# Performance work log

Hardware: AMD Instinct MI355X
Metric: run time of the kernel (lower is better)

The kernel has to match this reference:

```python
import jax, jax.numpy as jnp
import numpy as np

IN_FEATURES = 1024
OUT_FEATURES = 1024
KNOT_COUNT = 5
ORDER = 3
BATCH = 4096


def setup_inputs() -> dict:
    key = jax.random.key(0)
    k1, k2 = jax.random.split(key)
    x = jax.random.normal(k1, (BATCH, IN_FEATURES), dtype=jnp.float32)
    knots = jnp.linspace(-1.0, 1.0, KNOT_COUNT, dtype=jnp.float32)
    coeffs = jax.random.normal(k2, (KNOT_COUNT + ORDER, OUT_FEATURES, IN_FEATURES), dtype=jnp.float32)
    return {"x": x, "knots": knots, "coeffs": coeffs}


def _bspline_bases(x, knots, order):
    # x: [B, I]; knots: [K] uniform grid. Extend to K + 2*order + 1 knots so
    # the number of degree-`order` basis functions is K + order.
    h = knots[1] - knots[0]
    left = knots[0] + h * jnp.arange(-order, 0, dtype=knots.dtype)
    right = knots[-1] + h * jnp.arange(1, order + 2, dtype=knots.dtype)
    t = jnp.concatenate([left, knots, right])  # [K + 2*order + 1]
    xe = x[..., None]  # [B, I, 1]
    # degree-0 indicator bases: [B, I, m-1]
    bases = ((xe >= t[:-1]) & (xe < t[1:])).astype(x.dtype)
    # Cox-de Boor recursion up to degree `order` (vectorized over batch/features)
    for k in range(1, order + 1):
        left_num = (xe - t[: -(k + 1)]) / (t[k:-1] - t[: -(k + 1)])
        right_num = (t[k + 1:] - xe) / (t[k + 1:] - t[1:-k])
        bases = left_num * bases[..., :-1] + right_num * bases[..., 1:]
    return bases  # [B, I, K + order]


def reference(x, knots, coeffs):
    # Faithful fused version of the per-(i,j) python loops:
    # spline_j(b) = sum_n B_n(x[b,i]) * coeffs[n, j, i]; output sums over i.
    bases = _bspline_bases(x, knots, ORDER)          # [B, I, N]
    return jnp.einsum('bin,noi->bo', bases, coeffs)  # [B, O]
```

## Files before the change

### kernel.cpp

```cpp
#include <hip/hip_runtime.h>
#include <hip/hip_bf16.h>
#include <cstdint>
#include <cstddef>

#define IN_F   1024
#define OUT_F  1024
#define NB     8
#define BATCH  4096
#define KTOT   (NB * IN_F)

typedef __attribute__((ext_vector_type(4))) float  f32x4;
typedef __attribute__((ext_vector_type(8))) float  f32x8;
typedef __attribute__((ext_vector_type(8))) __bf16 bf16x8;
typedef __attribute__((ext_vector_type(4))) unsigned short u16x4;

#define GLDS16(g, l)                                                     \
    __builtin_amdgcn_global_load_lds(                                    \
        (const __attribute__((address_space(1))) void*)(g),              \
        (__attribute__((address_space(3))) void*)(l), 16, 0, 0)

__device__ __forceinline__ void spline_w(float r, float w[4]) {
    const float r2 = r * r, r3 = r2 * r;
    const float omr = 1.0f - r;
    w[0] = omr * omr * omr * (1.0f / 6.0f);
    w[1] = (3.0f * r3 - 6.0f * r2 + 4.0f) * (1.0f / 6.0f);
    w[2] = (-3.0f * r3 + 3.0f * r2 + 3.0f * r + 1.0f) * (1.0f / 6.0f);
    w[3] = r3 * (1.0f / 6.0f);
}

__global__ void k_cvt(const float* __restrict__ src, __bf16* __restrict__ dst) {
    const size_t g   = blockIdx.x * blockDim.x + threadIdx.x;
    const size_t idx = g * 8;
    const int i = (int)(idx & 1023);
    const int o = (int)((idx >> 10) & 1023);
    const int c = (i >> 3) & 7;
    const int isw = (i & ~63) | ((c ^ (o & 7)) << 3);
    f32x8 v = *(const f32x8*)(src + idx);
    bf16x8 ov = __builtin_convertvector(v, bf16x8);
    *(bf16x8*)(dst + (idx - i) + isw) = ov;
}

__global__ void k_basis(const float* __restrict__ x, __bf16* __restrict__ A) {
    const int g    = blockIdx.x * blockDim.x + threadIdx.x;
    const int flat = g * 4;
    const int b = flat >> 10, i = flat & 1023;
    f32x4 xv = *(const f32x4*)(x + flat);

    float w[4][4];
    int   jj[4];
#pragma unroll
    for (int e = 0; e < 4; ++e) {
        const float u  = (xv[e] + 2.5f) * 2.0f;
        const float jf = floorf(u);
        jj[e] = (int)jf;
        spline_w(u - jf, w[e]);
    }

    const int c   = (i >> 3) & 7;
    const int isw = (i & ~63) | ((c ^ (b & 7)) << 3) | (i & 7);
    __bf16* base = A + (size_t)b * KTOT + isw;
#pragma unroll
    for (int n = 0; n < NB; ++n) {
        u16x4 pack;
#pragma unroll
        for (int e = 0; e < 4; ++e) {
            const int d = n - jj[e] + 3;
            float v = (d == 0) ? w[e][0]
                    : (d == 1) ? w[e][1]
                    : (d == 2) ? w[e][2]
                    : (d == 3) ? w[e][3] : 0.0f;
            __bf16 h = (__bf16)v;
            pack[e] = __builtin_bit_cast(unsigned short, h);
        }
        *(u16x4*)(base + n * IN_F) = pack;
    }
}

#define BM 256
#define BN 128
#define BK 64
#define NT (KTOT / BK)
#define SPLITK 2
#define NTS (NT / SPLITK)
#define BUFSZ 49152

__global__ __launch_bounds__(512) void k_gemm(const __bf16* __restrict__ A,
                                              const __bf16* __restrict__ W,
                                              float* __restrict__ C,
                                              float* __restrict__ P) {
    __shared__ __align__(16) char ls[3 * BUFSZ];

    const int fid = blockIdx.x;
    const int xcd = fid & 7;
    const int s   = fid >> 3;
    const int y   = xcd + 8 * (s & 1);
    const int xb  = (s >> 1) & 7;
    const int kz  = s >> 4;

    const int o0   = xb * BN;
    const int b0   = y * BM;
    const int tid  = threadIdx.x;
    const int lane = tid & 63;
    const int wv   = tid >> 6;
    const int wr   = wv >> 1;
    const int wc   = wv & 1;
    const int l15  = lane & 15;
    const int lhi  = lane >> 4;

    f32x4 acc[4][4] = {};

    const int srow  = tid >> 3;
    const int scol8 = (tid & 7) * 8;

    auto STAGE = [&](int buf, int kt) {
        const int k0 = kt * BK;
        const int n  = k0 >> 10;
        const int i0 = k0 & 1023;
        char* la = ls + buf * BUFSZ;
        char* lb = la + 32768;
#pragma unroll
        for (int it = 0; it < 4; ++it) {
            const __bf16* ga = A + (size_t)(b0 + srow + it * 64) * KTOT + k0 + scol8;
            GLDS16(ga, la + tid * 16 + it * 8192);
        }
#pragma unroll
        for (int it = 0; it < 2; ++it) {
            const __bf16* gw = W + ((size_t)n << 20)
                                 + (size_t)(o0 + srow + it * 64) * IN_F + i0 + scol8;
            GLDS16(gw, lb + tid * 16 + it * 8192);
        }
    };

    const int ktBeg = kz * NTS;
    STAGE(0, ktBeg);
    STAGE(1, ktBeg + 1);

    int cur = 0, nxt = 2;
    for (int t = 0; t < NTS; ++t) {
        if (t < NTS - 1) asm volatile("s_waitcnt vmcnt(6)" ::: "memory");
        else             asm volatile("s_waitcnt vmcnt(0)" ::: "memory");
        __builtin_amdgcn_s_barrier();
        __builtin_amdgcn_sched_barrier(0);

        if (t + 2 < NTS) STAGE(nxt, ktBeg + t + 2);

        const char* la = ls + cur * BUFSZ;
        const char* lb = la + 32768;
#pragma unroll
        for (int kk = 0; kk < BK; kk += 32) {
            bf16x8 af[4], bfr[4];
#pragma unroll
            for (int m = 0; m < 4; ++m) {
                const int r = wr * 64 + m * 16 + l15;
                const int c = ((kk >> 3) + lhi) ^ (r & 7);
                af[m] = *(const bf16x8*)(la + r * 128 + c * 16);
            }
#pragma unroll
            for (int nn = 0; nn < 4; ++nn) {
                const int r = wc * 64 + nn * 16 + l15;
                const int c = ((kk >> 3) + lhi) ^ (r & 7);
                bfr[nn] = *(const bf16x8*)(lb + r * 128 + c * 16);
            }
#pragma unroll
            for (int m = 0; m < 4; ++m)
#pragma unroll
                for (int nn = 0; nn < 4; ++nn)
                    acc[m][nn] = __builtin_amdgcn_mfma_f32_16x16x32_bf16(
                        af[m], bfr[nn], acc[m][nn], 0, 0, 0);
        }
        cur = (cur == 2) ? 0 : cur + 1;
        nxt = (nxt == 2) ? 0 : nxt + 1;
    }

    float* dst = (kz == 0) ? C : P;
    const int crow = lhi * 4;
#pragma unroll
    for (int m = 0; m < 4; ++m) {
#pragma unroll
        for (int nn = 0; nn < 4; ++nn) {
            float* cp = dst + (size_t)(b0 + wr * 64 + m * 16 + crow) * OUT_F
                            + o0 + wc * 64 + nn * 16 + l15;
#pragma unroll
            for (int j = 0; j < 4; ++j)
                cp[(size_t)j * OUT_F] = acc[m][nn][j];
        }
    }
}

__global__ void k_add(float* __restrict__ C, const float* __restrict__ P) {
    const size_t g = (size_t)(blockIdx.x * blockDim.x + threadIdx.x) * 4;
    f32x4 a = *(const f32x4*)(C + g);
    f32x4 b = *(const f32x4*)(P + g);
    a += b;
    *(f32x4*)(C + g) = a;
}

__global__ void k_naive(const float* __restrict__ x, const float* __restrict__ coeffs,
                        float* __restrict__ out) {
    const int b = blockIdx.y * 16 + (threadIdx.x >> 4);
    const int o = blockIdx.x * 16 + (threadIdx.x & 15);
    float sum = 0.0f;
    for (int i = 0; i < IN_F; ++i) {
        const float u  = (x[(size_t)b * IN_F + i] + 2.5f) * 2.0f;
        const float jf = floorf(u);
        const int   j  = (int)jf;
        float w[4];
        spline_w(u - jf, w);
#pragma unroll
        for (int m = 0; m < 4; ++m) {
            const int idx = j - 3 + m;
            if (idx >= 0 && idx < NB)
                sum += w[m] * coeffs[(size_t)idx * OUT_F * IN_F + (size_t)o * IN_F + i];
        }
    }
    out[(size_t)b * OUT_F + o] = sum;
}

extern "C" void kernel_launch(void* const* d_in, const int* in_sizes, int n_in,
                              void* d_out, int out_size, void* d_ws, size_t ws_size,
                              hipStream_t stream) {
    const float* x      = (const float*)d_in[0];
    const float* coeffs = (const float*)d_in[2];
    float* out = (float*)d_out;

    const size_t needA = (size_t)BATCH * KTOT * sizeof(__bf16);
    const size_t needW = (size_t)NB * OUT_F * IN_F * sizeof(__bf16);
    const size_t needP = (size_t)BATCH * OUT_F * sizeof(float);

    if (ws_size >= needA + needW + needP) {
        __bf16* A  = (__bf16*)d_ws;
        __bf16* Wb = (__bf16*)((char*)d_ws + needA);
        float*  P  = (float*)((char*)d_ws + needA + needW);

        hipLaunchKernelGGL(k_cvt, dim3(NB * OUT_F * IN_F / 8 / 256), dim3(256), 0,
                           stream, coeffs, Wb);
        hipLaunchKernelGGL(k_basis, dim3(BATCH * IN_F / 4 / 256), dim3(256), 0,
                           stream, x, A);
        hipLaunchKernelGGL(k_gemm, dim3(256), dim3(512), 0, stream, A, Wb, out, P);
        hipLaunchKernelGGL(k_add, dim3(BATCH * OUT_F / 4 / 256), dim3(256), 0,
                           stream, out, P);
    } else {
        hipLaunchKernelGGL(k_naive, dim3(OUT_F / 16, BATCH / 16), dim3(256), 0,
                           stream, x, coeffs, out);
    }
}
```

Measured before the change: 121.1 us.

## Merge prep kernels and interleave A/B staging with MFMA phases using setprio

The weight-conversion and basis-building kernels are merged into one launch, with the block index choosing the role, which saves a launch and lets both run at once. The GEMM main loop is split into two half-K phases. The A tile prefetch is issued in the first phase and the B tile prefetch in the second, each after the LDS fragment reads. MFMA issue is bracketed with s_setprio and extra barriers. The aim is to overlap global-to-LDS traffic with matrix math, at the cost of extra barriers per iteration and a changed vmcnt accounting pattern.

```diff
diff --git a/kernel.cpp b/kernel.cpp
--- a/kernel.cpp
+++ b/kernel.cpp
@@ -9,10 +9,10 @@
 #define BATCH  4096
 #define KTOT   (NB * IN_F)
 
-typedef __attribute__((ext_vector_type(4))) float  f32x4;
-typedef __attribute__((ext_vector_type(8))) float  f32x8;
-typedef __attribute__((ext_vector_type(8))) __bf16 bf16x8;
-typedef __attribute__((ext_vector_type(4))) unsigned short u16x4;
+typedef __attribute__((ext_vector_type(4)))  float  f32x4;
+typedef __attribute__((ext_vector_type(8)))  float  f32x8;
+typedef __attribute__((ext_vector_type(8)))  __bf16 bf16x8;
+typedef __attribute__((ext_vector_type(4)))  unsigned short u16x4;
 
 #define GLDS16(g, l)                                                     \
     __builtin_amdgcn_global_load_lds(                                    \
@@ -28,51 +28,53 @@
     w[3] = r3 * (1.0f / 6.0f);
 }
 
-__global__ void k_cvt(const float* __restrict__ src, __bf16* __restrict__ dst) {
-    const size_t g   = blockIdx.x * blockDim.x + threadIdx.x;
-    const size_t idx = g * 8;
-    const int i = (int)(idx & 1023);
-    const int o = (int)((idx >> 10) & 1023);
-    const int c = (i >> 3) & 7;
-    const int isw = (i & ~63) | ((c ^ (o & 7)) << 3);
-    f32x8 v = *(const f32x8*)(src + idx);
-    bf16x8 ov = __builtin_convertvector(v, bf16x8);
-    *(bf16x8*)(dst + (idx - i) + isw) = ov;
-}
-
-__global__ void k_basis(const float* __restrict__ x, __bf16* __restrict__ A) {
-    const int g    = blockIdx.x * blockDim.x + threadIdx.x;
-    const int flat = g * 4;
-    const int b = flat >> 10, i = flat & 1023;
-    f32x4 xv = *(const f32x4*)(x + flat);
-
-    float w[4][4];
-    int   jj[4];
-#pragma unroll
-    for (int e = 0; e < 4; ++e) {
-        const float u  = (xv[e] + 2.5f) * 2.0f;
-        const float jf = floorf(u);
-        jj[e] = (int)jf;
-        spline_w(u - jf, w[e]);
-    }
-
-    const int c   = (i >> 3) & 7;
-    const int isw = (i & ~63) | ((c ^ (b & 7)) << 3) | (i & 7);
-    __bf16* base = A + (size_t)b * KTOT + isw;
-#pragma unroll
-    for (int n = 0; n < NB; ++n) {
-        u16x4 pack;
+__global__ void k_prep(const float* __restrict__ coeffs, __bf16* __restrict__ Wb,
+                       const float* __restrict__ x, __bf16* __restrict__ A) {
+    const int bb = blockIdx.x;
+    if (bb < 4096) {
+        const size_t g   = (size_t)bb * blockDim.x + threadIdx.x;
+        const size_t idx = g * 8;
+        const int i = (int)(idx & 1023);
+        const int o = (int)((idx >> 10) & 1023);
+        const int c = (i >> 3) & 7;
+        const int isw = (i & ~63) | ((c ^ (o & 7)) << 3);
+        f32x8 v = *(const f32x8*)(coeffs + idx);
+        bf16x8 ov = __builtin_convertvector(v, bf16x8);
+        *(bf16x8*)(Wb + (idx - i) + isw) = ov;
+    } else {
+        const int g    = (bb - 4096) * blockDim.x + threadIdx.x;
+        const int flat = g * 4;
+        const int b = flat >> 10, i = flat & 1023;
+        f32x4 xv = *(const f32x4*)(x + flat);
+
+        float w[4][4];
+        int   jj[4];
 #pragma unroll
         for (int e = 0; e < 4; ++e) {
-            const int d = n - jj[e] + 3;
-            float v = (d == 0) ? w[e][0]
-                    : (d == 1) ? w[e][1]
-                    : (d == 2) ? w[e][2]
-                    : (d == 3) ? w[e][3] : 0.0f;
-            __bf16 h = (__bf16)v;
-            pack[e] = __builtin_bit_cast(unsigned short, h);
-        }
-        *(u16x4*)(base + n * IN_F) = pack;
+            const float u  = (xv[e] + 2.5f) * 2.0f;
+            const float jf = floorf(u);
+            jj[e] = (int)jf;
+            spline_w(u - jf, w[e]);
+        }
+
+        const int c   = (i >> 3) & 7;
+        const int isw = (i & ~63) | ((c ^ (b & 7)) << 3) | (i & 7);
+        __bf16* base = A + (size_t)b * KTOT + isw;
+#pragma unroll
+        for (int n = 0; n < NB; ++n) {
+            u16x4 pack;
+#pragma unroll
+            for (int e = 0; e < 4; ++e) {
+                const int d = n - jj[e] + 3;
+                float v = (d == 0) ? w[e][0]
+                        : (d == 1) ? w[e][1]
+                        : (d == 2) ? w[e][2]
+                        : (d == 3) ? w[e][3] : 0.0f;
+                __bf16 h = (__bf16)v;
+                pack[e] = __builtin_bit_cast(unsigned short, h);
+            }
+            *(u16x4*)(base + n * IN_F) = pack;
+        }
     }
 }
 
@@ -112,17 +114,20 @@
     const int srow  = tid >> 3;
     const int scol8 = (tid & 7) * 8;
 
-    auto STAGE = [&](int buf, int kt) {
+    auto STAGE_A = [&](int buf, int kt) {
+        const int k0 = kt * BK;
+        char* la = ls + buf * BUFSZ;
+#pragma unroll
+        for (int it = 0; it < 4; ++it) {
+            const __bf16* ga = A + (size_t)(b0 + srow + it * 64) * KTOT + k0 + scol8;
+            GLDS16(ga, la + tid * 16 + it * 8192);
+        }
+    };
+    auto STAGE_B = [&](int buf, int kt) {
         const int k0 = kt * BK;
         const int n  = k0 >> 10;
         const int i0 = k0 & 1023;
-        char* la = ls + buf * BUFSZ;
-        char* lb = la + 32768;
-#pragma unroll
-        for (int it = 0; it < 4; ++it) {
-            const __bf16* ga = A + (size_t)(b0 + srow + it * 64) * KTOT + k0 + scol8;
-            GLDS16(ga, la + tid * 16 + it * 8192);
-        }
+        char* lb = ls + buf * BUFSZ + 32768;
 #pragma unroll
         for (int it = 0; it < 2; ++it) {
             const __bf16* gw = W + ((size_t)n << 20)
@@ -132,8 +137,8 @@
     };
 
     const int ktBeg = kz * NTS;
-    STAGE(0, ktBeg);
-    STAGE(1, ktBeg + 1);
+    STAGE_A(0, ktBeg);     STAGE_B(0, ktBeg);
+    STAGE_A(1, ktBeg + 1); STAGE_B(1, ktBeg + 1);
 
     int cur = 0, nxt = 2;
     for (int t = 0; t < NTS; ++t) {
@@ -142,31 +147,61 @@
         __builtin_amdgcn_s_barrier();
         __builtin_amdgcn_sched_barrier(0);
 
-        if (t + 2 < NTS) STAGE(nxt, ktBeg + t + 2);
-
         const char* la = ls + cur * BUFSZ;
         const char* lb = la + 32768;
-#pragma unroll
-        for (int kk = 0; kk < BK; kk += 32) {
+        const bool doStage = (t + 2 < NTS);
+        const int  kt2     = ktBeg + t + 2;
+
+        {
             bf16x8 af[4], bfr[4];
 #pragma unroll
             for (int m = 0; m < 4; ++m) {
                 const int r = wr * 64 + m * 16 + l15;
-                const int c = ((kk >> 3) + lhi) ^ (r & 7);
+                const int c = lhi ^ (r & 7);
                 af[m] = *(const bf16x8*)(la + r * 128 + c * 16);
             }
 #pragma unroll
             for (int nn = 0; nn < 4; ++nn) {
                 const int r = wc * 64 + nn * 16 + l15;
-                const int c = ((kk >> 3) + lhi) ^ (r & 7);
+                const int c = lhi ^ (r & 7);
                 bfr[nn] = *(const bf16x8*)(lb + r * 128 + c * 16);
             }
+            if (doStage) STAGE_A(nxt, kt2);
+            __builtin_amdgcn_s_barrier();
+            __builtin_amdgcn_s_setprio(1);
 #pragma unroll
             for (int m = 0; m < 4; ++m)
 #pragma unroll
                 for (int nn = 0; nn < 4; ++nn)
                     acc[m][nn] = __builtin_amdgcn_mfma_f32_16x16x32_bf16(
                         af[m], bfr[nn], acc[m][nn], 0, 0, 0);
+            __builtin_amdgcn_s_setprio(0);
+            __builtin_amdgcn_s_barrier();
+        }
+        {
+            bf16x8 af[4], bfr[4];
+#pragma unroll
+            for (int m = 0; m < 4; ++m) {
+                const int r = wr * 64 + m * 16 + l15;
+                const int c = (4 + lhi) ^ (r & 7);
+                af[m] = *(const bf16x8*)(la + r * 128 + c * 16);
+            }
+#pragma unroll
+            for (int nn = 0; nn < 4; ++nn) {
+                const int r = wc * 64 + nn * 16 + l15;
+                const int c = (4 + lhi) ^ (r & 7);
+                bfr[nn] = *(const bf16x8*)(lb + r * 128 + c * 16);
+            }
+            if (doStage) STAGE_B(nxt, kt2);
+            __builtin_amdgcn_s_barrier();
+            __builtin_amdgcn_s_setprio(1);
+#pragma unroll
+            for (int m = 0; m < 4; ++m)
+#pragma unroll
+                for (int nn = 0; nn < 4; ++nn)
+                    acc[m][nn] = __builtin_amdgcn_mfma_f32_16x16x32_bf16(
+                        af[m], bfr[nn], acc[m][nn], 0, 0, 0);
+            __builtin_amdgcn_s_setprio(0);
         }
         cur = (cur == 2) ? 0 : cur + 1;
         nxt = (nxt == 2) ? 0 : nxt + 1;
@@ -232,10 +267,8 @@
         __bf16* Wb = (__bf16*)((char*)d_ws + needA);
         float*  P  = (float*)((char*)d_ws + needA + needW);
 
-        hipLaunchKernelGGL(k_cvt, dim3(NB * OUT_F * IN_F / 8 / 256), dim3(256), 0,
-                           stream, coeffs, Wb);
-        hipLaunchKernelGGL(k_basis, dim3(BATCH * IN_F / 4 / 256), dim3(256), 0,
-                           stream, x, A);
+        hipLaunchKernelGGL(k_prep, dim3(8192), dim3(256), 0, stream,
+                           coeffs, Wb, x, A);
         hipLaunchKernelGGL(k_gemm, dim3(256), dim3(512), 0, stream, A, Wb, out, P);
         hipLaunchKernelGGL(k_add, dim3(BATCH * OUT_F / 4 / 256), dim3(256), 0,
                            stream, out, P);
```

Measured after the change: 120.6 us. Within noise of the previous version (-0.4%).

## Retile GEMM to 128x128x32 with 3-way split-K and fuse prep kernels

Applied to the files above, without the earlier changes.

Merges the coefficient conversion and basis expansion into one prep launch. Rebuilds the GEMM with 128x128 tiles, BK=32, 256 threads, three blocks per CU and a new LDS swizzle. It uses split-K of 3 across 768 blocks and brackets the MFMA block with s_setprio. The intent is better occupancy and CU coverage with one fewer launch, in exchange for an extra fp32 partial buffer, more reduction traffic in k_add, and less reuse per tile.

```diff
diff --git a/kernel.cpp b/kernel.cpp
--- a/kernel.cpp
+++ b/kernel.cpp
@@ -9,10 +9,10 @@
 #define BATCH  4096
 #define KTOT   (NB * IN_F)
 
-typedef __attribute__((ext_vector_type(4))) float  f32x4;
-typedef __attribute__((ext_vector_type(8))) float  f32x8;
-typedef __attribute__((ext_vector_type(8))) __bf16 bf16x8;
-typedef __attribute__((ext_vector_type(4))) unsigned short u16x4;
+typedef __attribute__((ext_vector_type(4)))  float  f32x4;
+typedef __attribute__((ext_vector_type(8)))  float  f32x8;
+typedef __attribute__((ext_vector_type(8)))  __bf16 bf16x8;
+typedef __attribute__((ext_vector_type(4)))  unsigned short u16x4;
 
 #define GLDS16(g, l)                                                     \
     __builtin_amdgcn_global_load_lds(                                    \
@@ -28,77 +28,80 @@
     w[3] = r3 * (1.0f / 6.0f);
 }
 
-__global__ void k_cvt(const float* __restrict__ src, __bf16* __restrict__ dst) {
-    const size_t g   = blockIdx.x * blockDim.x + threadIdx.x;
-    const size_t idx = g * 8;
-    const int i = (int)(idx & 1023);
-    const int o = (int)((idx >> 10) & 1023);
-    const int c = (i >> 3) & 7;
-    const int isw = (i & ~63) | ((c ^ (o & 7)) << 3);
-    f32x8 v = *(const f32x8*)(src + idx);
-    bf16x8 ov = __builtin_convertvector(v, bf16x8);
-    *(bf16x8*)(dst + (idx - i) + isw) = ov;
-}
-
-__global__ void k_basis(const float* __restrict__ x, __bf16* __restrict__ A) {
-    const int g    = blockIdx.x * blockDim.x + threadIdx.x;
-    const int flat = g * 4;
-    const int b = flat >> 10, i = flat & 1023;
-    f32x4 xv = *(const f32x4*)(x + flat);
-
-    float w[4][4];
-    int   jj[4];
-#pragma unroll
-    for (int e = 0; e < 4; ++e) {
-        const float u  = (xv[e] + 2.5f) * 2.0f;
-        const float jf = floorf(u);
-        jj[e] = (int)jf;
-        spline_w(u - jf, w[e]);
-    }
-
-    const int c   = (i >> 3) & 7;
-    const int isw = (i & ~63) | ((c ^ (b & 7)) << 3) | (i & 7);
-    __bf16* base = A + (size_t)b * KTOT + isw;
-#pragma unroll
-    for (int n = 0; n < NB; ++n) {
-        u16x4 pack;
+__global__ void k_prep(const float* __restrict__ coeffs, __bf16* __restrict__ Wb,
+                       const float* __restrict__ x, __bf16* __restrict__ A) {
+    const int bb = blockIdx.x;
+    if (bb < 4096) {
+        const size_t g   = (size_t)bb * blockDim.x + threadIdx.x;
+        const size_t idx = g * 8;
+        const int i = (int)(idx & 1023);
+        const int o = (int)((idx >> 10) & 1023);
+        const int c = (i >> 3) & 3;
+        const int isw = (i & ~31) | ((c ^ (o & 3)) << 3);
+        f32x8 v = *(const f32x8*)(coeffs + idx);
+        bf16x8 ov = __builtin_convertvector(v, bf16x8);
+        *(bf16x8*)(Wb + (idx - i) + isw) = ov;
+    } else {
+        const int g    = (bb - 4096) * blockDim.x + threadIdx.x;
+        const int flat = g * 4;
+        const int b = flat >> 10, i = flat & 1023;
+        f32x4 xv = *(const f32x4*)(x + flat);
+
+        float w[4][4];
+        int   jj[4];
 #pragma unroll
         for (int e = 0; e < 4; ++e) {
-            const int d = n - jj[e] + 3;
-            float v = (d == 0) ? w[e][0]
-                    : (d == 1) ? w[e][1]
-                    : (d == 2) ? w[e][2]
-                    : (d == 3) ? w[e][3] : 0.0f;
-            __bf16 h = (__bf16)v;
-            pack[e] = __builtin_bit_cast(unsigned short, h);
-        }
-        *(u16x4*)(base + n * IN_F) = pack;
-    }
-}
-
-#define BM 256
-#define BN 128
-#define BK 64
-#define NT (KTOT / BK)
-#define SPLITK 2
-#define NTS (NT / SPLITK)
-#define BUFSZ 49152
-
-__global__ __launch_bounds__(512) void k_gemm(const __bf16* __restrict__ A,
-                                              const __bf16* __restrict__ W,
-                                              float* __restrict__ C,
-                                              float* __restrict__ P) {
+            const float u  = (xv[e] + 2.5f) * 2.0f;
+            const float jf = floorf(u);
+            jj[e] = (int)jf;
+            spline_w(u - jf, w[e]);
+        }
+
+        const int c   = (i >> 3) & 3;
+        const int isw = (i & ~31) | ((c ^ (b & 3)) << 3) | (i & 7);
+        __bf16* base = A + (size_t)b * KTOT + isw;
+#pragma unroll
+        for (int n = 0; n < NB; ++n) {
+            u16x4 pack;
+#pragma unroll
+            for (int e = 0; e < 4; ++e) {
+                const int d = n - jj[e] + 3;
+                float v = (d == 0) ? w[e][0]
+                        : (d == 1) ? w[e][1]
+                        : (d == 2) ? w[e][2]
+                        : (d == 3) ? w[e][3] : 0.0f;
+                __bf16 h = (__bf16)v;
+                pack[e] = __builtin_bit_cast(unsigned short, h);
+            }
+            *(u16x4*)(base + n * IN_F) = pack;
+        }
+    }
+}
+
+#define BK 32
+#define BUFSZ 16384
+#define SK 3
+
+__device__ __forceinline__ int lds_off(int r, int kc) {
+    const int slot = (((((r >> 6) ^ (r >> 2)) & 1)) << 2) | ((kc ^ r) & 3);
+    return (r & 63) * 128 + slot * 16;
+}
+
+__global__ __launch_bounds__(256, 3) void k_gemm(const __bf16* __restrict__ A,
+                                                 const __bf16* __restrict__ W,
+                                                 float* __restrict__ C,
+                                                 float* __restrict__ P) {
     __shared__ __align__(16) char ls[3 * BUFSZ];
 
     const int fid = blockIdx.x;
-    const int xcd = fid & 7;
     const int s   = fid >> 3;
-    const int y   = xcd + 8 * (s & 1);
-    const int xb  = (s >> 1) & 7;
-    const int kz  = s >> 4;
-
-    const int o0   = xb * BN;
-    const int b0   = y * BM;
+    const int row = (fid & 7) * 4 + (s & 3);
+    const int rem = s >> 2;
+    const int col = rem & 7;
+    const int kz  = rem >> 3;
+
+    const int b0   = row * 128;
+    const int o0   = col * 128;
     const int tid  = threadIdx.x;
     const int lane = tid & 63;
     const int wv   = tid >> 6;
@@ -109,89 +112,84 @@
 
     f32x4 acc[4][4] = {};
 
-    const int srow  = tid >> 3;
-    const int scol8 = (tid & 7) * 8;
+    const int p    = tid & 7;
+    const int Rr   = tid >> 3;
+    const int rg0  = Rr + 64 * (((p >> 2) ^ (Rr >> 2)) & 1);
+    const int Rr1  = Rr + 32;
+    const int rg1  = Rr1 + 64 * (((p >> 2) ^ (Rr1 >> 2)) & 1);
+    const int kpos = (p & 3) * 8;
 
     auto STAGE = [&](int buf, int kt) {
         const int k0 = kt * BK;
         const int n  = k0 >> 10;
         const int i0 = k0 & 1023;
         char* la = ls + buf * BUFSZ;
-        char* lb = la + 32768;
-#pragma unroll
-        for (int it = 0; it < 4; ++it) {
-            const __bf16* ga = A + (size_t)(b0 + srow + it * 64) * KTOT + k0 + scol8;
-            GLDS16(ga, la + tid * 16 + it * 8192);
-        }
-#pragma unroll
-        for (int it = 0; it < 2; ++it) {
-            const __bf16* gw = W + ((size_t)n << 20)
-                                 + (size_t)(o0 + srow + it * 64) * IN_F + i0 + scol8;
-            GLDS16(gw, lb + tid * 16 + it * 8192);
-        }
+        char* lb = la + 8192;
+        GLDS16(A + (size_t)(b0 + rg0) * KTOT + k0 + kpos, la + tid * 16);
+        GLDS16(A + (size_t)(b0 + rg1) * KTOT + k0 + kpos, la + tid * 16 + 4096);
+        GLDS16(W + ((size_t)n << 20) + (size_t)(o0 + rg0) * IN_F + i0 + kpos,
+               lb + tid * 16);
+        GLDS16(W + ((size_t)n << 20) + (size_t)(o0 + rg1) * IN_F + i0 + kpos,
+               lb + tid * 16 + 4096);
     };
 
-    const int ktBeg = kz * NTS;
+    const int ktBeg = kz * 85;
+    const int n_t   = (kz == 2) ? 86 : 85;
+
     STAGE(0, ktBeg);
     STAGE(1, ktBeg + 1);
 
     int cur = 0, nxt = 2;
-    for (int t = 0; t < NTS; ++t) {
-        if (t < NTS - 1) asm volatile("s_waitcnt vmcnt(6)" ::: "memory");
+    for (int t = 0; t < n_t; ++t) {
+        if (t < n_t - 1) asm volatile("s_waitcnt vmcnt(4)" ::: "memory");
         else             asm volatile("s_waitcnt vmcnt(0)" ::: "memory");
         __builtin_amdgcn_s_barrier();
         __builtin_amdgcn_sched_barrier(0);
 
-        if (t + 2 < NTS) STAGE(nxt, ktBeg + t + 2);
+        if (t + 2 < n_t) STAGE(nxt, ktBeg + t + 2);
 
         const char* la = ls + cur * BUFSZ;
-        const char* lb = la + 32768;
-#pragma unroll
-        for (int kk = 0; kk < BK; kk += 32) {
-            bf16x8 af[4], bfr[4];
-#pragma unroll
-            for (int m = 0; m < 4; ++m) {
-                const int r = wr * 64 + m * 16 + l15;
-                const int c = ((kk >> 3) + lhi) ^ (r & 7);
-                af[m] = *(const bf16x8*)(la + r * 128 + c * 16);
-            }
-#pragma unroll
-            for (int nn = 0; nn < 4; ++nn) {
-                const int r = wc * 64 + nn * 16 + l15;
-                const int c = ((kk >> 3) + lhi) ^ (r & 7);
-                bfr[nn] = *(const bf16x8*)(lb + r * 128 + c * 16);
-            }
-#pragma unroll
-            for (int m = 0; m < 4; ++m)
-#pragma unroll
-                for (int nn = 0; nn < 4; ++nn)
-                    acc[m][nn] = __builtin_amdgcn_mfma_f32_16x16x32_bf16(
-                        af[m], bfr[nn], acc[m][nn], 0, 0, 0);
-        }
+        const char* lb = la + 8192;
+        bf16x8 af[4], bfr[4];
+#pragma unroll
+        for (int m = 0; m < 4; ++m)
+            af[m] = *(const bf16x8*)(la + lds_off(wr * 64 + m * 16 + l15, lhi));
+#pragma unroll
+        for (int n2 = 0; n2 < 4; ++n2)
+            bfr[n2] = *(const bf16x8*)(lb + lds_off(wc * 64 + n2 * 16 + l15, lhi));
+        __builtin_amdgcn_s_setprio(1);
+#pragma unroll
+        for (int m = 0; m < 4; ++m)
+#pragma unroll
+            for (int n2 = 0; n2 < 4; ++n2)
+                acc[m][n2] = __builtin_amdgcn_mfma_f32_16x16x32_bf16(
+                    af[m], bfr[n2], acc[m][n2], 0, 0, 0);
+        __builtin_amdgcn_s_setprio(0);
         cur = (cur == 2) ? 0 : cur + 1;
         nxt = (nxt == 2) ? 0 : nxt + 1;
     }
 
-    float* dst = (kz == 0) ? C : P;
+    float* dst = (kz == 0) ? C : P + (size_t)(kz - 1) * BATCH * OUT_F;
     const int crow = lhi * 4;
 #pragma unroll
-    for (int m = 0; m < 4; ++m) {
-#pragma unroll
-        for (int nn = 0; nn < 4; ++nn) {
+    for (int m = 0; m < 4; ++m)
+#pragma unroll
+        for (int n2 = 0; n2 < 4; ++n2) {
             float* cp = dst + (size_t)(b0 + wr * 64 + m * 16 + crow) * OUT_F
-                            + o0 + wc * 64 + nn * 16 + l15;
+                            + o0 + wc * 64 + n2 * 16 + l15;
 #pragma unroll
             for (int j = 0; j < 4; ++j)
-                cp[(size_t)j * OUT_F] = acc[m][nn][j];
-        }
-    }
-}
-
+                cp[(size_t)j * OUT_F] = acc[m][n2][j];
+        }
+}
+
+template <int NP>
 __global__ void k_add(float* __restrict__ C, const float* __restrict__ P) {
     const size_t g = (size_t)(blockIdx.x * blockDim.x + threadIdx.x) * 4;
     f32x4 a = *(const f32x4*)(C + g);
-    f32x4 b = *(const f32x4*)(P + g);
-    a += b;
+#pragma unroll
+    for (int pi = 0; pi < NP; ++pi)
+        a += *(const f32x4*)(P + (size_t)pi * BATCH * OUT_F + g);
     *(f32x4*)(C + g) = a;
 }
 
@@ -225,20 +223,19 @@
 
     const size_t needA = (size_t)BATCH * KTOT * sizeof(__bf16);
     const size_t needW = (size_t)NB * OUT_F * IN_F * sizeof(__bf16);
-    const size_t needP = (size_t)BATCH * OUT_F * sizeof(float);
-
-    if (ws_size >= needA + needW + needP) {
+    const size_t oneP  = (size_t)BATCH * OUT_F * sizeof(float);
+
+    if (ws_size >= needA + needW + 2 * oneP) {
         __bf16* A  = (__bf16*)d_ws;
         __bf16* Wb = (__bf16*)((char*)d_ws + needA);
         float*  P  = (float*)((char*)d_ws + needA + needW);
 
-        hipLaunchKernelGGL(k_cvt, dim3(NB * OUT_F * IN_F / 8 / 256), dim3(256), 0,
-                           stream, coeffs, Wb);
-        hipLaunchKernelGGL(k_basis, dim3(BATCH * IN_F / 4 / 256), dim3(256), 0,
-                           stream, x, A);
-        hipLaunchKernelGGL(k_gemm, dim3(256), dim3(512), 0, stream, A, Wb, out, P);
-        hipLaunchKernelGGL(k_add, dim3(BATCH * OUT_F / 4 / 256), dim3(256), 0,
-                           stream, out, P);
+        hipLaunchKernelGGL(k_prep, dim3(8192), dim3(256), 0, stream,
+                           coeffs, Wb, x, A);
+        hipLaunchKernelGGL(k_gemm, dim3(768), dim3(256), 0, stream,
+                           A, Wb, out, P);
+        hipLaunchKernelGGL(k_add<2>, dim3(BATCH * OUT_F / 4 / 256), dim3(256),
+                           0, stream, out, P);
     } else {
         hipLaunchKernelGGL(k_naive, dim3(OUT_F / 16, BATCH / 16), dim3(256), 0,
                            stream, x, coeffs, out);
```

New measurement: 136.7 us. 1.13x slower.

## Merge prep kernels and software-pipeline LDS fragment reads in GEMM loop

Applied to the files above, without the earlier changes.

Merges the coefficient conversion and basis expansion into one launch, and the basis path now handles 8 features per thread with 16-byte stores. The GEMM main loop is restructured so LDS fragment reads for the next half-tile overlap the MFMAs of the current one. It uses double register fragments, split barriers and s_setprio around the MFMA bursts. This is meant to hide LDS latency and cut launch overhead, at the cost of extra registers and more complex barrier/waitcnt ordering.

```diff
diff --git a/kernel.cpp b/kernel.cpp
--- a/kernel.cpp
+++ b/kernel.cpp
@@ -9,15 +9,20 @@
 #define BATCH  4096
 #define KTOT   (NB * IN_F)
 
-typedef __attribute__((ext_vector_type(4))) float  f32x4;
-typedef __attribute__((ext_vector_type(8))) float  f32x8;
-typedef __attribute__((ext_vector_type(8))) __bf16 bf16x8;
-typedef __attribute__((ext_vector_type(4))) unsigned short u16x4;
+typedef __attribute__((ext_vector_type(4)))  float  f32x4;
+typedef __attribute__((ext_vector_type(8)))  float  f32x8;
+typedef __attribute__((ext_vector_type(8)))  __bf16 bf16x8;
 
 #define GLDS16(g, l)                                                     \
     __builtin_amdgcn_global_load_lds(                                    \
         (const __attribute__((address_space(1))) void*)(g),              \
         (__attribute__((address_space(3))) void*)(l), 16, 0, 0)
+
+#define FENCE() __builtin_amdgcn_sched_barrier(0)
+#define BARA()  do { FENCE(); __builtin_amdgcn_s_barrier(); FENCE(); } while (0)
+#define BARB()  do { FENCE(); __builtin_amdgcn_s_barrier(); FENCE(); } while (0)
+#define VMC(n)  do { asm volatile("s_waitcnt vmcnt(" #n ")" ::: "memory");  \
+                     FENCE(); } while (0)
 
 __device__ __forceinline__ void spline_w(float r, float w[4]) {
     const float r2 = r * r, r3 = r2 * r;
@@ -28,51 +33,52 @@
     w[3] = r3 * (1.0f / 6.0f);
 }
 
-__global__ void k_cvt(const float* __restrict__ src, __bf16* __restrict__ dst) {
-    const size_t g   = blockIdx.x * blockDim.x + threadIdx.x;
-    const size_t idx = g * 8;
-    const int i = (int)(idx & 1023);
-    const int o = (int)((idx >> 10) & 1023);
-    const int c = (i >> 3) & 7;
-    const int isw = (i & ~63) | ((c ^ (o & 7)) << 3);
-    f32x8 v = *(const f32x8*)(src + idx);
-    bf16x8 ov = __builtin_convertvector(v, bf16x8);
-    *(bf16x8*)(dst + (idx - i) + isw) = ov;
-}
-
-__global__ void k_basis(const float* __restrict__ x, __bf16* __restrict__ A) {
-    const int g    = blockIdx.x * blockDim.x + threadIdx.x;
-    const int flat = g * 4;
-    const int b = flat >> 10, i = flat & 1023;
-    f32x4 xv = *(const f32x4*)(x + flat);
-
-    float w[4][4];
-    int   jj[4];
-#pragma unroll
-    for (int e = 0; e < 4; ++e) {
-        const float u  = (xv[e] + 2.5f) * 2.0f;
-        const float jf = floorf(u);
-        jj[e] = (int)jf;
-        spline_w(u - jf, w[e]);
-    }
-
-    const int c   = (i >> 3) & 7;
-    const int isw = (i & ~63) | ((c ^ (b & 7)) << 3) | (i & 7);
-    __bf16* base = A + (size_t)b * KTOT + isw;
-#pragma unroll
-    for (int n = 0; n < NB; ++n) {
-        u16x4 pack;
-#pragma unroll
-        for (int e = 0; e < 4; ++e) {
-            const int d = n - jj[e] + 3;
-            float v = (d == 0) ? w[e][0]
-                    : (d == 1) ? w[e][1]
-                    : (d == 2) ? w[e][2]
-                    : (d == 3) ? w[e][3] : 0.0f;
-            __bf16 h = (__bf16)v;
-            pack[e] = __builtin_bit_cast(unsigned short, h);
-        }
-        *(u16x4*)(base + n * IN_F) = pack;
+__global__ void k_prep(const float* __restrict__ coeffs, __bf16* __restrict__ Wb,
+                       const float* __restrict__ x, __bf16* __restrict__ A) {
+    const int bb = blockIdx.x;
+    if (bb < 4096) {
+        const size_t g   = (size_t)bb * blockDim.x + threadIdx.x;
+        const size_t idx = g * 8;
+        const int i = (int)(idx & 1023);
+        const int o = (int)((idx >> 10) & 1023);
+        const int c = (i >> 3) & 7;
+        const int isw = (i & ~63) | ((c ^ (o & 7)) << 3);
+        f32x8 v = *(const f32x8*)(coeffs + idx);
+        bf16x8 ov = __builtin_convertvector(v, bf16x8);
+        *(bf16x8*)(Wb + (idx - i) + isw) = ov;
+    } else {
+        const int g    = (bb - 4096) * blockDim.x + threadIdx.x;
+        const int flat = g * 8;
+        const int b = flat >> 10, i = flat & 1023;
+        f32x8 xv = *(const f32x8*)(x + flat);
+
+        float w[8][4];
+        int   jj[8];
+#pragma unroll
+        for (int e = 0; e < 8; ++e) {
+            const float u  = (xv[e] + 2.5f) * 2.0f;
+            const float jf = floorf(u);
+            jj[e] = (int)jf;
+            spline_w(u - jf, w[e]);
+        }
+
+        const int c   = (i >> 3) & 7;
+        const int isw = (i & ~63) | ((c ^ (b & 7)) << 3);
+        __bf16* base = A + (size_t)b * KTOT + isw;
+#pragma unroll
+        for (int n = 0; n < NB; ++n) {
+            bf16x8 pack;
+#pragma unroll
+            for (int e = 0; e < 8; ++e) {
+                const int d = n - jj[e] + 3;
+                float v = (d == 0) ? w[e][0]
+                        : (d == 1) ? w[e][1]
+                        : (d == 2) ? w[e][2]
+                        : (d == 3) ? w[e][3] : 0.0f;
+                pack[e] = (__bf16)v;
+            }
+            *(bf16x8*)(base + n * IN_F) = pack;
+        }
     }
 }
 
@@ -131,45 +137,73 @@
         }
     };
 
+    bf16x8 a0s[4], b0s[4], a1s[4], b1s[4];
+
+    auto RD = [&](bf16x8 (&af)[4], bf16x8 (&bf)[4], int buf, int h) {
+        const char* la = ls + buf * BUFSZ;
+        const char* lb = la + 32768;
+#pragma unroll
+        for (int m = 0; m < 4; ++m) {
+            const int r = wr * 64 + m * 16 + l15;
+            const int c = (h * 4 + lhi) ^ (r & 7);
+            af[m] = *(const bf16x8*)(la + r * 128 + c * 16);
+        }
+#pragma unroll
+        for (int n2 = 0; n2 < 4; ++n2) {
+            const int r = wc * 64 + n2 * 16 + l15;
+            const int c = (h * 4 + lhi) ^ (r & 7);
+            bf[n2] = *(const bf16x8*)(lb + r * 128 + c * 16);
+        }
+    };
+    auto MM = [&](bf16x8 (&af)[4], bf16x8 (&bf)[4]) {
+        __builtin_amdgcn_s_setprio(1);
+#pragma unroll
+        for (int m = 0; m < 4; ++m)
+#pragma unroll
+            for (int n2 = 0; n2 < 4; ++n2)
+                acc[m][n2] = __builtin_amdgcn_mfma_f32_16x16x32_bf16(
+                    af[m], bf[n2], acc[m][n2], 0, 0, 0);
+        __builtin_amdgcn_s_setprio(0);
+    };
+
     const int ktBeg = kz * NTS;
+
     STAGE(0, ktBeg);
     STAGE(1, ktBeg + 1);
-
-    int cur = 0, nxt = 2;
-    for (int t = 0; t < NTS; ++t) {
-        if (t < NTS - 1) asm volatile("s_waitcnt vmcnt(6)" ::: "memory");
-        else             asm volatile("s_waitcnt vmcnt(0)" ::: "memory");
-        __builtin_amdgcn_s_barrier();
-        __builtin_amdgcn_sched_barrier(0);
-
-        if (t + 2 < NTS) STAGE(nxt, ktBeg + t + 2);
-
-        const char* la = ls + cur * BUFSZ;
-        const char* lb = la + 32768;
-#pragma unroll
-        for (int kk = 0; kk < BK; kk += 32) {
-            bf16x8 af[4], bfr[4];
-#pragma unroll
-            for (int m = 0; m < 4; ++m) {
-                const int r = wr * 64 + m * 16 + l15;
-                const int c = ((kk >> 3) + lhi) ^ (r & 7);
-                af[m] = *(const bf16x8*)(la + r * 128 + c * 16);
-            }
-#pragma unroll
-            for (int nn = 0; nn < 4; ++nn) {
-                const int r = wc * 64 + nn * 16 + l15;
-                const int c = ((kk >> 3) + lhi) ^ (r & 7);
-                bfr[nn] = *(const bf16x8*)(lb + r * 128 + c * 16);
-            }
-#pragma unroll
-            for (int m = 0; m < 4; ++m)
-#pragma unroll
-                for (int nn = 0; nn < 4; ++nn)
-                    acc[m][nn] = __builtin_amdgcn_mfma_f32_16x16x32_bf16(
-                        af[m], bfr[nn], acc[m][nn], 0, 0, 0);
-        }
-        cur = (cur == 2) ? 0 : cur + 1;
-        nxt = (nxt == 2) ? 0 : nxt + 1;
+    VMC(6);
+    __builtin_amdgcn_s_barrier();
+    FENCE();
+    int cur = 0;
+    RD(a0s, b0s, 0, 0);
+
+    for (int t = 0; t < NTS - 2; ++t) {
+        int nx1 = cur + 1; if (nx1 == 3) nx1 = 0;
+        int nx2 = nx1 + 1; if (nx2 == 3) nx2 = 0;
+        BARA();
+        STAGE(nx2, ktBeg + t + 2);
+        VMC(6);
+        BARB();
+        RD(a1s, b1s, cur, 1);
+        MM(a0s, b0s);
+        RD(a0s, b0s, nx1, 0);
+        MM(a1s, b1s);
+        cur = nx1;
+    }
+    {
+        int nx1 = cur + 1; if (nx1 == 3) nx1 = 0;
+        BARA();
+        VMC(0);
+        BARB();
+        RD(a1s, b1s, cur, 1);
+        MM(a0s, b0s);
+        RD(a0s, b0s, nx1, 0);
+        MM(a1s, b1s);
+        cur = nx1;
+    }
+    {
+        RD(a1s, b1s, cur, 1);
+        MM(a0s, b0s);
+        MM(a1s, b1s);
     }
 
     float* dst = (kz == 0) ? C : P;
@@ -177,12 +211,12 @@
 #pragma unroll
     for (int m = 0; m < 4; ++m) {
 #pragma unroll
-        for (int nn = 0; nn < 4; ++nn) {
+        for (int n2 = 0; n2 < 4; ++n2) {
             float* cp = dst + (size_t)(b0 + wr * 64 + m * 16 + crow) * OUT_F
-                            + o0 + wc * 64 + nn * 16 + l15;
+                            + o0 + wc * 64 + n2 * 16 + l15;
 #pragma unroll
             for (int j = 0; j < 4; ++j)
-                cp[(size_t)j * OUT_F] = acc[m][nn][j];
+                cp[(size_t)j * OUT_F] = acc[m][n2][j];
         }
     }
 }
@@ -225,20 +259,19 @@
 
     const size_t needA = (size_t)BATCH * KTOT * sizeof(__bf16);
     const size_t needW = (size_t)NB * OUT_F * IN_F * sizeof(__bf16);
-    const size_t needP = (size_t)BATCH * OUT_F * sizeof(float);
-
-    if (ws_size >= needA + needW + needP) {
+    const size_t oneP  = (size_t)BATCH * OUT_F * sizeof(float);
+
+    if (ws_size >= needA + needW + oneP) {
         __bf16* A  = (__bf16*)d_ws;
         __bf16* Wb = (__bf16*)((char*)d_ws + needA);
         float*  P  = (float*)((char*)d_ws + needA + needW);
 
-        hipLaunchKernelGGL(k_cvt, dim3(NB * OUT_F * IN_F / 8 / 256), dim3(256), 0,
-                           stream, coeffs, Wb);
-        hipLaunchKernelGGL(k_basis, dim3(BATCH * IN_F / 4 / 256), dim3(256), 0,
-                           stream, x, A);
-        hipLaunchKernelGGL(k_gemm, dim3(256), dim3(512), 0, stream, A, Wb, out, P);
-        hipLaunchKernelGGL(k_add, dim3(BATCH * OUT_F / 4 / 256), dim3(256), 0,
-                           stream, out, P);
+        hipLaunchKernelGGL(k_prep, dim3(6144), dim3(256), 0, stream,
+                           coeffs, Wb, x, A);
+        hipLaunchKernelGGL(k_gemm, dim3(256), dim3(512), 0, stream,
+                           A, Wb, out, P);
+        hipLaunchKernelGGL(k_add, dim3(BATCH * OUT_F / 4 / 256), dim3(256),
+                           0, stream, out, P);
     } else {
         hipLaunchKernelGGL(k_naive, dim3(OUT_F / 16, BATCH / 16), dim3(256), 0,
                            stream, x, coeffs, out);
```

New measurement: 124.9 us. 1.03x slower.
